# Optimization experiments

Measured on AMD Instinct MI355X. Metric: run time of the kernel, lower is better.

## Reference

```python
import jax, jax.numpy as jnp
import numpy as np

B, C, D = 64, 1000, 2048
SCALE_CONF = 10.0   # confidence scale in forward
SCALE_COS = 16.0    # CosNorm_Classifier default scale


def setup_inputs() -> dict:
    key = jax.random.key(0)
    ks = jax.random.split(key, 8)
    x = jax.random.normal(ks[0], (B, D), jnp.float32)
    labels = jax.random.randint(ks[1], (B,), 0, C)
    centers = jax.random.normal(ks[2], (C, D), jnp.float32)
    class_count = jax.random.randint(ks[3], (C,), 0, 100)
    # learned parameters
    fc_channel_w = jax.random.normal(ks[4], (D, D), jnp.float32) * 0.02
    fc_channel_b = jnp.zeros((D,), jnp.float32)
    fc1_w = jax.random.normal(ks[5], (C, D), jnp.float32) * 0.02
    fc1_b = jnp.zeros((C,), jnp.float32)
    cos_w = jax.random.normal(ks[6], (C, D), jnp.float32) * 0.001
    return {"x": x, "labels": labels, "centers": centers, "class_count": class_count,
            "fc_channel_w": fc_channel_w, "fc_channel_b": fc_channel_b,
            "fc1_w": fc1_w, "fc1_b": fc1_b, "cos_w": cos_w}


def reference(x, labels, centers, class_count, fc_channel_w, fc_channel_b, fc1_w, fc1_b, cos_w):
    # pairwise L2 distance to all class centers; only the per-row min is used
    # downstream, so we fuse the sort-then-take-first into a min reduction.
    x2 = jnp.sum(x * x, axis=1, keepdims=True)            # [B,1]
    c2 = jnp.sum(centers * centers, axis=1)               # [C]
    d2 = jnp.maximum(x2 - 2.0 * (x @ centers.T) + c2[None, :], 0.0)  # [B,C]
    min_dist = jnp.sqrt(jnp.min(d2, axis=1, keepdims=True))          # [B,1] == values_nn[:,0]
    confidence = SCALE_CONF / min_dist                    # broadcasts over feat dim

    # stage-1 classifier -> soft assignment to centers (memory hallucination)
    logits_stage1 = x @ fc1_w.T + fc1_b                   # [B,C]
    prob_stage1 = jax.nn.softmax(logits_stage1, axis=1)
    centers_cur = prob_stage1 @ centers                   # [B,D]

    channel_selector = jnp.tanh(x @ fc_channel_w.T + fc_channel_b)  # [B,D]
    slow_feature = x
    fast_feature = channel_selector * centers_cur
    x_new = confidence * (x + fast_feature)               # [B,D]

    # CosNorm_Classifier: ex = (|x|/(1+|x|)) * x/|x|; ew = w/|w|; logits = scale*ex @ ew.T
    norm_x = jnp.linalg.norm(x_new, axis=1, keepdims=True)
    ex = (norm_x / (1.0 + norm_x)) * (x_new / norm_x)
    ew = cos_w / jnp.linalg.norm(cos_w, axis=1, keepdims=True)
    logits = (SCALE_COS * ex) @ ew.T                      # [B,C]

    return logits, slow_feature, fast_feature
```

## Files before the change

### kernel.cpp

```cpp
#include <hip/hip_runtime.h>
#include <hip/hip_bf16.h>
#include <math.h>

typedef __attribute__((ext_vector_type(8))) short short8;
typedef __attribute__((ext_vector_type(4))) float f32x4;

#define MFMA(a, b, c) __builtin_amdgcn_mfma_f32_16x16x32_bf16(a, b, c, 0, 0, 0)

enum : int {
  WS_XB    = 0,
  WS_X2    = 65536,
  WS_DMINP = 65600,
  WS_SPART = 69696,
  WS_PROB  = 73792,
  WS_SEL   = 106560,
  WS_XNB   = 172096,
  WS_XN2P  = 237632,
  WS_P5    = 245824,
};

__device__ inline short bfs(float f) {
  __hip_bfloat16 h = __float2bfloat16(f);
  return __builtin_bit_cast(short, h);
}
__device__ inline float bf2f(unsigned short u) {
  return __uint_as_float((unsigned)u << 16);
}

__device__ inline void gload16(const float* g, float* lds) {
  __builtin_amdgcn_global_load_lds(
      (const __attribute__((address_space(1))) unsigned int*)g,
      (__attribute__((address_space(3))) unsigned int*)lds, 16, 0, 0);
}

__global__ __launch_bounds__(256) void k1(const float* __restrict__ x,
                                          float* __restrict__ out,
                                          float* __restrict__ ws) {
  __shared__ float red[4];
  int b = blockIdx.x, t = threadIdx.x;
  int l = t & 63, w = t >> 6;
  const float* xr = x + (size_t)b * 2048 + t * 8;
  float4 f0 = *(const float4*)(xr);
  float4 f1 = *(const float4*)(xr + 4);
  short8 h;
  h[0] = bfs(f0.x); h[1] = bfs(f0.y); h[2] = bfs(f0.z); h[3] = bfs(f0.w);
  h[4] = bfs(f1.x); h[5] = bfs(f1.y); h[6] = bfs(f1.z); h[7] = bfs(f1.w);
  *(short8*)((unsigned short*)(ws + WS_XB) + (size_t)b * 2048 + t * 8) = h;
  *(float4*)(out + 64000 + (size_t)b * 2048 + t * 8) = f0;
  *(float4*)(out + 64000 + (size_t)b * 2048 + t * 8 + 4) = f1;
  float s = f0.x*f0.x + f0.y*f0.y + f0.z*f0.z + f0.w*f0.w
          + f1.x*f1.x + f1.y*f1.y + f1.z*f1.z + f1.w*f1.w;
#pragma unroll
  for (int o = 32; o; o >>= 1) s += __shfl_xor(s, o);
  if (l == 0) red[w] = s;
  __syncthreads();
  if (t == 0) ws[WS_X2 + b] = red[0] + red[1] + red[2] + red[3];
}

__global__ __launch_bounds__(512) void k2(const float* __restrict__ centers,
                                          const float* __restrict__ fc1w,
                                          const float* __restrict__ fcw,
                                          const float* __restrict__ fc1b,
                                          const float* __restrict__ fcb,
                                          float* __restrict__ ws) {
  __shared__ float WT[2][16][1028];
  __shared__ f32x4 sacc[8][64];
  __shared__ float ssq[8][64];
  int blk = blockIdx.x, t = threadIdx.x;
  int w = t >> 6, l = t & 63;
  int ln = l & 15, lk = l >> 4;
  int n0 = blk * 16;
  bool cen = (n0 < 1024);

  auto stage = [&](int buf, int koff) {
    for (int r = 0; r < 2; ++r) {
      int row = w * 2 + r;
      int n = n0 + row;
      const float* brow;
      if (n < 1024)      brow = centers + (size_t)min(n, 999) * 2048;
      else if (n < 2048) brow = fc1w + (size_t)min(n - 1024, 999) * 2048;
      else               brow = fcw + (size_t)(n - 2048) * 2048;
#pragma unroll
      for (int j = 0; j < 4; ++j)
        gload16(brow + koff + j * 256 + l * 4, &WT[buf][row][j * 256]);
    }
  };

  stage(0, 0);
  __syncthreads();
  stage(1, 1024);

  int m0 = (w & 3) * 16;
  int kq = (w >> 2) * 512;
  const unsigned short* aptr =
      (const unsigned short*)(ws + WS_XB) + (size_t)(m0 + ln) * 2048 + kq + lk * 8;
  f32x4 acc = {0.f, 0.f, 0.f, 0.f};
  float sq = 0.f;

  {
    const float* wrow = &WT[0][ln][kq + lk * 8];
#pragma unroll 4
    for (int ks = 0; ks < 16; ++ks) {
      short8 a0 = *(const short8*)(aptr + ks * 32);
      float4 f0 = *(const float4*)(wrow + ks * 32);
      float4 f1 = *(const float4*)(wrow + ks * 32 + 4);
      if (cen)
        sq += f0.x*f0.x + f0.y*f0.y + f0.z*f0.z + f0.w*f0.w
            + f1.x*f1.x + f1.y*f1.y + f1.z*f1.z + f1.w*f1.w;
      short8 bb;
      bb[0] = bfs(f0.x); bb[1] = bfs(f0.y); bb[2] = bfs(f0.z); bb[3] = bfs(f0.w);
      bb[4] = bfs(f1.x); bb[5] = bfs(f1.y); bb[6] = bfs(f1.z); bb[7] = bfs(f1.w);
      acc = MFMA(a0, bb, acc);
    }
  }
  __syncthreads();
  {
    const float* wrow = &WT[1][ln][kq + lk * 8];
    const unsigned short* ap1 = aptr + 1024;
#pragma unroll 4
    for (int ks = 0; ks < 16; ++ks) {
      short8 a0 = *(const short8*)(ap1 + ks * 32);
      float4 f0 = *(const float4*)(wrow + ks * 32);
      float4 f1 = *(const float4*)(wrow + ks * 32 + 4);
      if (cen)
        sq += f0.x*f0.x + f0.y*f0.y + f0.z*f0.z + f0.w*f0.w
            + f1.x*f1.x + f1.y*f1.y + f1.z*f1.z + f1.w*f1.w;
      short8 bb;
      bb[0] = bfs(f0.x); bb[1] = bfs(f0.y); bb[2] = bfs(f0.z); bb[3] = bfs(f0.w);
      bb[4] = bfs(f1.x); bb[5] = bfs(f1.y); bb[6] = bfs(f1.z); bb[7] = bfs(f1.w);
      acc = MFMA(a0, bb, acc);
    }
  }

  sacc[w][l] = acc;
  ssq[w][l] = sq;
  __syncthreads();
  if (w < 4) {
    f32x4 a2 = sacc[w + 4][l];
    acc.x += a2.x; acc.y += a2.y; acc.z += a2.z; acc.w += a2.w;
    sq = ssq[w][l] + ssq[w + 4][l];

    if (cen) {
      sq += __shfl_xor(sq, 16);
      sq += __shfl_xor(sq, 32);
      int colv = n0 + ln;
#pragma unroll
      for (int j = 0; j < 4; ++j) {
        int m = m0 + lk * 4 + j;
        float d2 = (colv < 1000)
            ? fmaxf(ws[WS_X2 + m] - 2.f * acc[j] + sq, 0.f) : 3.0e38f;
        d2 = fminf(d2, __shfl_xor(d2, 1));
        d2 = fminf(d2, __shfl_xor(d2, 2));
        d2 = fminf(d2, __shfl_xor(d2, 4));
        d2 = fminf(d2, __shfl_xor(d2, 8));
        if (ln == 0) ws[WS_DMINP + blk * 64 + m] = d2;
      }
    } else if (n0 < 2048) {
      int c = n0 - 1024 + ln;
      unsigned short* pb = (unsigned short*)(ws + WS_PROB);
#pragma unroll
      for (int j = 0; j < 4; ++j) {
        int m = m0 + lk * 4 + j;
        float e = (c < 1000) ? __expf(acc[j] + fc1b[c]) : 0.f;
        pb[(size_t)m * 1024 + c] = (unsigned short)bfs(e);
        float s = e;
        s += __shfl_xor(s, 1);
        s += __shfl_xor(s, 2);
        s += __shfl_xor(s, 4);
        s += __shfl_xor(s, 8);
        if (ln == 0) ws[WS_SPART + (blk - 64) * 64 + m] = s;
      }
    } else {
      int d = n0 - 2048 + ln;
      unsigned short* sel = (unsigned short*)(ws + WS_SEL);
#pragma unroll
      for (int j = 0; j < 4; ++j) {
        int m = m0 + lk * 4 + j;
        float sv = tanhf(acc[j] + fcb[d]);
        sel[(size_t)m * 2048 + d] = (unsigned short)bfs(sv);
      }
    }
  }
}

__global__ __launch_bounds__(256) void kde(const float* __restrict__ centers,
                                           const float* __restrict__ x,
                                           float* __restrict__ out,
                                           float* __restrict__ ws) {
  __shared__ f32x4 sacc[4][2][64];
  __shared__ float sinv[64];
  int blk = blockIdx.x, t = threadIdx.x;
  int w = t >> 6, l = t & 63;
  int cs = blk >> 1, mh = blk & 1;
  int d0 = cs * 16, m0 = mh * 32;
  int ln = l & 15, lk = l >> 4;
  int k0 = w * 256;
  if (t < 64) {
    float s = 0.f;
#pragma unroll
    for (int i = 0; i < 64; ++i) s += ws[WS_SPART + i * 64 + t];
    sinv[t] = 1.0f / s;
  }
  const unsigned short* aptr =
      (const unsigned short*)(ws + WS_PROB) + (size_t)(m0 + ln) * 1024 + k0 + lk * 8;
  f32x4 acc0 = {0.f, 0.f, 0.f, 0.f}, acc1 = {0.f, 0.f, 0.f, 0.f};
  for (int ks = 0; ks < 8; ++ks) {
    short8 a0 = *(const short8*)(aptr + ks * 32);
    short8 a1 = *(const short8*)(aptr + 16 * 1024 + ks * 32);
    int kbase = k0 + ks * 32 + lk * 8;
    short8 bb;
#pragma unroll
    for (int j = 0; j < 8; ++j) {
      int kc = min(kbase + j, 999);
      bb[j] = bfs(centers[(size_t)kc * 2048 + d0 + ln]);
    }
    acc0 = MFMA(a0, bb, acc0);
    acc1 = MFMA(a1, bb, acc1);
  }
  sacc[w][0][l] = acc0;
  sacc[w][1][l] = acc1;
  __syncthreads();
  if (w == 0) {
    f32x4 r0 = sacc[0][0][l], r1 = sacc[0][1][l];
#pragma unroll
    for (int i = 1; i < 4; ++i) {
      f32x4 u0 = sacc[i][0][l], u1 = sacc[i][1][l];
      r0.x += u0.x; r0.y += u0.y; r0.z += u0.z; r0.w += u0.w;
      r1.x += u1.x; r1.y += u1.y; r1.z += u1.z; r1.w += u1.w;
    }
    const unsigned short* sel = (const unsigned short*)(ws + WS_SEL);
    unsigned short* xnb = (unsigned short*)(ws + WS_XNB);
    float rr[8] = {r0.x, r0.y, r0.z, r0.w, r1.x, r1.y, r1.z, r1.w};
#pragma unroll
    for (int q = 0; q < 8; ++q) {
      int b = m0 + (q >> 2) * 16 + lk * 4 + (q & 3);
      int d = d0 + ln;
      float cc = rr[q] * sinv[b];
      float sv = bf2f(sel[(size_t)b * 2048 + d]);
      float xv = x[(size_t)b * 2048 + d];
      float fast = sv * cc;
      out[195072 + (size_t)b * 2048 + d] = fast;
      float yv = xv + fast;
      xnb[(size_t)b * 2048 + d] = (unsigned short)bfs(yv);
      float sq = yv * yv;
      sq += __shfl_xor(sq, 1);
      sq += __shfl_xor(sq, 2);
      sq += __shfl_xor(sq, 4);
      sq += __shfl_xor(sq, 8);
      if (ln == 0) ws[WS_XN2P + cs * 64 + b] = sq;
    }
  }
}

__global__ __launch_bounds__(256) void k7(const float* __restrict__ cosw,
                                          float* __restrict__ ws) {
  int blk = blockIdx.x, t = threadIdx.x;
  int w = t >> 6, l = t & 63;
  int colblk = blk & 31, ksplit = blk >> 5;
  int ln = l & 15, lk = l >> 4;
  int n = colblk * 32 + (w & 1) * 16 + ln;
  int m0 = (w >> 1) * 32;
  int k0 = ksplit * 512;
  const float* bptr = cosw + (size_t)min(n, 999) * 2048 + k0 + lk * 8;
  const unsigned short* aptr =
      (const unsigned short*)(ws + WS_XNB) + (size_t)(m0 + ln) * 2048 + k0 + lk * 8;
  f32x4 acc0 = {0.f, 0.f, 0.f, 0.f}, acc1 = {0.f, 0.f, 0.f, 0.f};
  float sq = 0.f;
#pragma unroll 4
  for (int ks = 0; ks < 16; ++ks) {
    short8 a0 = *(const short8*)(aptr + ks * 32);
    short8 a1 = *(const short8*)(aptr + 16 * 2048 + ks * 32);
    float4 f0 = *(const float4*)(bptr + ks * 32);
    float4 f1 = *(const float4*)(bptr + ks * 32 + 4);
    sq += f0.x*f0.x + f0.y*f0.y + f0.z*f0.z + f0.w*f0.w
        + f1.x*f1.x + f1.y*f1.y + f1.z*f1.z + f1.w*f1.w;
    short8 bb;
    bb[0] = bfs(f0.x); bb[1] = bfs(f0.y); bb[2] = bfs(f0.z); bb[3] = bfs(f0.w);
    bb[4] = bfs(f1.x); bb[5] = bfs(f1.y); bb[6] = bfs(f1.z); bb[7] = bfs(f1.w);
    acc0 = MFMA(a0, bb, acc0);
    acc1 = MFMA(a1, bb, acc1);
  }
  float* P = ws + WS_P5 + ((size_t)ksplit * 1024 + n) * 68;
  *(f32x4*)(P + m0 + lk * 4) = acc0;
  *(f32x4*)(P + m0 + 16 + lk * 4) = acc1;
  sq += __shfl_xor(sq, 16);
  sq += __shfl_xor(sq, 32);
  if (w < 2 && l < 16) P[64] = sq;
}

__global__ __launch_bounds__(256) void k8(float* __restrict__ out,
                                          const float* __restrict__ ws) {
  __shared__ float tile[64][65];
  __shared__ float scale[64];
  int blk = blockIdx.x, t = threadIdx.x, l = t & 63, w = t >> 6;
  int c0 = blk * 64;
  const size_t KS = (size_t)1024 * 68;
  if (t < 64) {
    float s = 0.f;
    for (int i = 0; i < 128; ++i) s += ws[WS_XN2P + i * 64 + t];
    float ny = sqrtf(fmaxf(s, 0.f));
    float d2 = 3.0e38f;
    for (int i = 0; i < 64; ++i) d2 = fminf(d2, ws[WS_DMINP + i * 64 + t]);
    float cf = 10.0f * rsqrtf(fmaxf(d2, 1e-20f));
    scale[t] = 16.0f * cf / (1.0f + cf * ny);
  }
  __syncthreads();
  for (int cl = w; cl < 64; cl += 4) {
    int c = c0 + cl;
    const float* P = ws + WS_P5 + (size_t)c * 68;
    float v = P[l] + P[KS + l] + P[2*KS + l] + P[3*KS + l];
    float w2 = P[64] + P[KS + 64] + P[2*KS + 64] + P[3*KS + 64];
    tile[cl][l] = v * rsqrtf(fmaxf(w2, 1e-30f)) * scale[l];
  }
  __syncthreads();
  for (int r = 0; r < 16; ++r) {
    int b = w * 16 + r;
    int c = c0 + l;
    if (c < 1000) out[(size_t)b * 1000 + c] = tile[l][b];
  }
}

extern "C" void kernel_launch(void* const* d_in, const int* in_sizes, int n_in,
                              void* d_out, int out_size, void* d_ws, size_t ws_size,
                              hipStream_t stream) {
  const float* x       = (const float*)d_in[0];
  const float* centers = (const float*)d_in[2];
  const float* fcw     = (const float*)d_in[4];
  const float* fcb     = (const float*)d_in[5];
  const float* fc1w    = (const float*)d_in[6];
  const float* fc1b    = (const float*)d_in[7];
  const float* cosw    = (const float*)d_in[8];
  float* out = (float*)d_out;
  float* ws  = (float*)d_ws;

  hipLaunchKernelGGL(k1,  dim3(64),  dim3(256), 0, stream, x, out, ws);
  hipLaunchKernelGGL(k2,  dim3(256), dim3(512), 0, stream, centers, fc1w, fcw, fc1b, fcb, ws);
  hipLaunchKernelGGL(kde, dim3(256), dim3(256), 0, stream, centers, x, out, ws);
  hipLaunchKernelGGL(k7,  dim3(128), dim3(256), 0, stream, cosw, ws);
  hipLaunchKernelGGL(k8,  dim3(16),  dim3(256), 0, stream, out, ws);
}
```

Baseline: 67.27 us.

## Pre-transpose centers to bf16 and fuse cosine classifier split-K with finalize

k1 gains extra blocks that transpose the centers matrix into a bf16 [D][1024] buffer. kde can then load contiguous short8 B fragments instead of doing eight strided scalar fp32 loads with a conversion per element. The cosine-classifier GEMM is restructured to 64 blocks of 512 threads that stage cos_w rows in LDS through global_load_lds. Split-K is reduced inside each block and the normalized, scaled logits are written directly, which removes the k8 kernel and its partial-sum buffer. The cost is a transpose pass over centers and fewer, larger blocks in k7.

Result: faster. 58.65 us (-12.8%).

```diff
diff --git a/kernel.cpp b/kernel.cpp
--- a/kernel.cpp
+++ b/kernel.cpp
@@ -16,7 +16,7 @@
   WS_SEL   = 106560,
   WS_XNB   = 172096,
   WS_XN2P  = 237632,
-  WS_P5    = 245824,
+  WS_CTB   = 245824,
 };
 
 __device__ inline short bfs(float f) {
@@ -34,27 +34,46 @@
 }
 
 __global__ __launch_bounds__(256) void k1(const float* __restrict__ x,
+                                          const float* __restrict__ centers,
                                           float* __restrict__ out,
                                           float* __restrict__ ws) {
-  __shared__ float red[4];
-  int b = blockIdx.x, t = threadIdx.x;
+  __shared__ float A[64][65];
+  int blk = blockIdx.x, t = threadIdx.x;
   int l = t & 63, w = t >> 6;
-  const float* xr = x + (size_t)b * 2048 + t * 8;
-  float4 f0 = *(const float4*)(xr);
-  float4 f1 = *(const float4*)(xr + 4);
-  short8 h;
-  h[0] = bfs(f0.x); h[1] = bfs(f0.y); h[2] = bfs(f0.z); h[3] = bfs(f0.w);
-  h[4] = bfs(f1.x); h[5] = bfs(f1.y); h[6] = bfs(f1.z); h[7] = bfs(f1.w);
-  *(short8*)((unsigned short*)(ws + WS_XB) + (size_t)b * 2048 + t * 8) = h;
-  *(float4*)(out + 64000 + (size_t)b * 2048 + t * 8) = f0;
-  *(float4*)(out + 64000 + (size_t)b * 2048 + t * 8 + 4) = f1;
-  float s = f0.x*f0.x + f0.y*f0.y + f0.z*f0.z + f0.w*f0.w
-          + f1.x*f1.x + f1.y*f1.y + f1.z*f1.z + f1.w*f1.w;
-#pragma unroll
-  for (int o = 32; o; o >>= 1) s += __shfl_xor(s, o);
-  if (l == 0) red[w] = s;
-  __syncthreads();
-  if (t == 0) ws[WS_X2 + b] = red[0] + red[1] + red[2] + red[3];
+  if (blk < 64) {
+    int b = blk;
+    const float* xr = x + (size_t)b * 2048 + t * 8;
+    float4 f0 = *(const float4*)(xr);
+    float4 f1 = *(const float4*)(xr + 4);
+    short8 h;
+    h[0] = bfs(f0.x); h[1] = bfs(f0.y); h[2] = bfs(f0.z); h[3] = bfs(f0.w);
+    h[4] = bfs(f1.x); h[5] = bfs(f1.y); h[6] = bfs(f1.z); h[7] = bfs(f1.w);
+    *(short8*)((unsigned short*)(ws + WS_XB) + (size_t)b * 2048 + t * 8) = h;
+    *(float4*)(out + 64000 + (size_t)b * 2048 + t * 8) = f0;
+    *(float4*)(out + 64000 + (size_t)b * 2048 + t * 8 + 4) = f1;
+    float s = f0.x*f0.x + f0.y*f0.y + f0.z*f0.z + f0.w*f0.w
+            + f1.x*f1.x + f1.y*f1.y + f1.z*f1.z + f1.w*f1.w;
+#pragma unroll
+    for (int o = 32; o; o >>= 1) s += __shfl_xor(s, o);
+    if (l == 0) A[0][w] = s;
+    __syncthreads();
+    if (t == 0) ws[WS_X2 + b] = A[0][0] + A[0][1] + A[0][2] + A[0][3];
+  } else {
+    int tid = blk - 64;
+    int tc = tid & 15, td = tid >> 4;
+    int c0 = tc * 64, d0 = td * 64;
+    for (int r = 0; r < 16; ++r) {
+      int cc = r * 4 + w;
+      int c = c0 + cc;
+      A[cc][l] = (c < 1000) ? centers[(size_t)c * 2048 + d0 + l] : 0.f;
+    }
+    __syncthreads();
+    unsigned short* ctb = (unsigned short*)(ws + WS_CTB);
+    for (int r = 0; r < 16; ++r) {
+      int dd = r * 4 + w;
+      ctb[(size_t)(d0 + dd) * 1024 + c0 + l] = (unsigned short)bfs(A[l][dd]);
+    }
+  }
 }
 
 __global__ __launch_bounds__(512) void k2(const float* __restrict__ centers,
@@ -183,8 +202,7 @@
   }
 }
 
-__global__ __launch_bounds__(256) void kde(const float* __restrict__ centers,
-                                           const float* __restrict__ x,
+__global__ __launch_bounds__(256) void kde(const float* __restrict__ x,
                                            float* __restrict__ out,
                                            float* __restrict__ ws) {
   __shared__ f32x4 sacc[4][2][64];
@@ -203,17 +221,14 @@
   }
   const unsigned short* aptr =
       (const unsigned short*)(ws + WS_PROB) + (size_t)(m0 + ln) * 1024 + k0 + lk * 8;
+  const unsigned short* brow =
+      (const unsigned short*)(ws + WS_CTB) + (size_t)(d0 + ln) * 1024 + k0 + lk * 8;
   f32x4 acc0 = {0.f, 0.f, 0.f, 0.f}, acc1 = {0.f, 0.f, 0.f, 0.f};
+#pragma unroll
   for (int ks = 0; ks < 8; ++ks) {
     short8 a0 = *(const short8*)(aptr + ks * 32);
     short8 a1 = *(const short8*)(aptr + 16 * 1024 + ks * 32);
-    int kbase = k0 + ks * 32 + lk * 8;
-    short8 bb;
-#pragma unroll
-    for (int j = 0; j < 8; ++j) {
-      int kc = min(kbase + j, 999);
-      bb[j] = bfs(centers[(size_t)kc * 2048 + d0 + ln]);
-    }
+    short8 bb = *(const short8*)(brow + ks * 32);
     acc0 = MFMA(a0, bb, acc0);
     acc1 = MFMA(a1, bb, acc1);
   }
@@ -252,49 +267,18 @@
   }
 }
 
-__global__ __launch_bounds__(256) void k7(const float* __restrict__ cosw,
+__global__ __launch_bounds__(512) void k7(const float* __restrict__ cosw,
+                                          float* __restrict__ out,
                                           float* __restrict__ ws) {
+  __shared__ float WT[2][16][1028];
+  __shared__ f32x4 sacc[8][64];
+  __shared__ float ssq[8][64];
+  __shared__ float scale_s[64];
   int blk = blockIdx.x, t = threadIdx.x;
   int w = t >> 6, l = t & 63;
-  int colblk = blk & 31, ksplit = blk >> 5;
   int ln = l & 15, lk = l >> 4;
-  int n = colblk * 32 + (w & 1) * 16 + ln;
-  int m0 = (w >> 1) * 32;
-  int k0 = ksplit * 512;
-  const float* bptr = cosw + (size_t)min(n, 999) * 2048 + k0 + lk * 8;
-  const unsigned short* aptr =
-      (const unsigned short*)(ws + WS_XNB) + (size_t)(m0 + ln) * 2048 + k0 + lk * 8;
-  f32x4 acc0 = {0.f, 0.f, 0.f, 0.f}, acc1 = {0.f, 0.f, 0.f, 0.f};
-  float sq = 0.f;
-#pragma unroll 4
-  for (int ks = 0; ks < 16; ++ks) {
-    short8 a0 = *(const short8*)(aptr + ks * 32);
-    short8 a1 = *(const short8*)(aptr + 16 * 2048 + ks * 32);
-    float4 f0 = *(const float4*)(bptr + ks * 32);
-    float4 f1 = *(const float4*)(bptr + ks * 32 + 4);
-    sq += f0.x*f0.x + f0.y*f0.y + f0.z*f0.z + f0.w*f0.w
-        + f1.x*f1.x + f1.y*f1.y + f1.z*f1.z + f1.w*f1.w;
-    short8 bb;
-    bb[0] = bfs(f0.x); bb[1] = bfs(f0.y); bb[2] = bfs(f0.z); bb[3] = bfs(f0.w);
-    bb[4] = bfs(f1.x); bb[5] = bfs(f1.y); bb[6] = bfs(f1.z); bb[7] = bfs(f1.w);
-    acc0 = MFMA(a0, bb, acc0);
-    acc1 = MFMA(a1, bb, acc1);
-  }
-  float* P = ws + WS_P5 + ((size_t)ksplit * 1024 + n) * 68;
-  *(f32x4*)(P + m0 + lk * 4) = acc0;
-  *(f32x4*)(P + m0 + 16 + lk * 4) = acc1;
-  sq += __shfl_xor(sq, 16);
-  sq += __shfl_xor(sq, 32);
-  if (w < 2 && l < 16) P[64] = sq;
-}
-
-__global__ __launch_bounds__(256) void k8(float* __restrict__ out,
-                                          const float* __restrict__ ws) {
-  __shared__ float tile[64][65];
-  __shared__ float scale[64];
-  int blk = blockIdx.x, t = threadIdx.x, l = t & 63, w = t >> 6;
-  int c0 = blk * 64;
-  const size_t KS = (size_t)1024 * 68;
+  int n0 = blk * 16;
+
   if (t < 64) {
     float s = 0.f;
     for (int i = 0; i < 128; ++i) s += ws[WS_XN2P + i * 64 + t];
@@ -302,21 +286,81 @@
     float d2 = 3.0e38f;
     for (int i = 0; i < 64; ++i) d2 = fminf(d2, ws[WS_DMINP + i * 64 + t]);
     float cf = 10.0f * rsqrtf(fmaxf(d2, 1e-20f));
-    scale[t] = 16.0f * cf / (1.0f + cf * ny);
-  }
-  __syncthreads();
-  for (int cl = w; cl < 64; cl += 4) {
-    int c = c0 + cl;
-    const float* P = ws + WS_P5 + (size_t)c * 68;
-    float v = P[l] + P[KS + l] + P[2*KS + l] + P[3*KS + l];
-    float w2 = P[64] + P[KS + 64] + P[2*KS + 64] + P[3*KS + 64];
-    tile[cl][l] = v * rsqrtf(fmaxf(w2, 1e-30f)) * scale[l];
-  }
-  __syncthreads();
-  for (int r = 0; r < 16; ++r) {
-    int b = w * 16 + r;
-    int c = c0 + l;
-    if (c < 1000) out[(size_t)b * 1000 + c] = tile[l][b];
+    scale_s[t] = 16.0f * cf / (1.0f + cf * ny);
+  }
+
+  auto stage = [&](int buf, int koff) {
+    for (int r = 0; r < 2; ++r) {
+      int row = w * 2 + r;
+      const float* brow = cosw + (size_t)min(n0 + row, 999) * 2048;
+#pragma unroll
+      for (int j = 0; j < 4; ++j)
+        gload16(brow + koff + j * 256 + l * 4, &WT[buf][row][j * 256]);
+    }
+  };
+
+  stage(0, 0);
+  __syncthreads();
+  stage(1, 1024);
+
+  int m0 = (w & 3) * 16;
+  int kq = (w >> 2) * 512;
+  const unsigned short* aptr =
+      (const unsigned short*)(ws + WS_XNB) + (size_t)(m0 + ln) * 2048 + kq + lk * 8;
+  f32x4 acc = {0.f, 0.f, 0.f, 0.f};
+  float sq = 0.f;
+
+  {
+    const float* wrow = &WT[0][ln][kq + lk * 8];
+#pragma unroll 4
+    for (int ks = 0; ks < 16; ++ks) {
+      short8 a0 = *(const short8*)(aptr + ks * 32);
+      float4 f0 = *(const float4*)(wrow + ks * 32);
+      float4 f1 = *(const float4*)(wrow + ks * 32 + 4);
+      sq += f0.x*f0.x + f0.y*f0.y + f0.z*f0.z + f0.w*f0.w
+          + f1.x*f1.x + f1.y*f1.y + f1.z*f1.z + f1.w*f1.w;
+      short8 bb;
+      bb[0] = bfs(f0.x); bb[1] = bfs(f0.y); bb[2] = bfs(f0.z); bb[3] = bfs(f0.w);
+      bb[4] = bfs(f1.x); bb[5] = bfs(f1.y); bb[6] = bfs(f1.z); bb[7] = bfs(f1.w);
+      acc = MFMA(a0, bb, acc);
+    }
+  }
+  __syncthreads();
+  {
+    const float* wrow = &WT[1][ln][kq + lk * 8];
+    const unsigned short* ap1 = aptr + 1024;
+#pragma unroll 4
+    for (int ks = 0; ks < 16; ++ks) {
+      short8 a0 = *(const short8*)(ap1 + ks * 32);
+      float4 f0 = *(const float4*)(wrow + ks * 32);
+      float4 f1 = *(const float4*)(wrow + ks * 32 + 4);
+      sq += f0.x*f0.x + f0.y*f0.y + f0.z*f0.z + f0.w*f0.w
+          + f1.x*f1.x + f1.y*f1.y + f1.z*f1.z + f1.w*f1.w;
+      short8 bb;
+      bb[0] = bfs(f0.x); bb[1] = bfs(f0.y); bb[2] = bfs(f0.z); bb[3] = bfs(f0.w);
+      bb[4] = bfs(f1.x); bb[5] = bfs(f1.y); bb[6] = bfs(f1.z); bb[7] = bfs(f1.w);
+      acc = MFMA(a0, bb, acc);
+    }
+  }
+
+  sacc[w][l] = acc;
+  ssq[w][l] = sq;
+  __syncthreads();
+  if (w < 4) {
+    f32x4 a2 = sacc[w + 4][l];
+    acc.x += a2.x; acc.y += a2.y; acc.z += a2.z; acc.w += a2.w;
+    sq = ssq[w][l] + ssq[w + 4][l];
+    sq += __shfl_xor(sq, 16);
+    sq += __shfl_xor(sq, 32);
+    float invw = rsqrtf(fmaxf(sq, 1e-30f));
+    int c = n0 + ln;
+    if (c < 1000) {
+#pragma unroll
+      for (int j = 0; j < 4; ++j) {
+        int m = m0 + lk * 4 + j;
+        out[(size_t)m * 1000 + c] = acc[j] * invw * scale_s[m];
+      }
+    }
   }
 }
 
@@ -333,9 +377,8 @@
   float* out = (float*)d_out;
   float* ws  = (float*)d_ws;
 
-  hipLaunchKernelGGL(k1,  dim3(64),  dim3(256), 0, stream, x, out, ws);
+  hipLaunchKernelGGL(k1,  dim3(576), dim3(256), 0, stream, x, centers, out, ws);
   hipLaunchKernelGGL(k2,  dim3(256), dim3(512), 0, stream, centers, fc1w, fcw, fc1b, fcb, ws);
-  hipLaunchKernelGGL(kde, dim3(256), dim3(256), 0, stream, centers, x, out, ws);
-  hipLaunchKernelGGL(k7,  dim3(128), dim3(256), 0, stream, cosw, ws);
-  hipLaunchKernelGGL(k8,  dim3(16),  dim3(256), 0, stream, out, ws);
-}
+  hipLaunchKernelGGL(kde, dim3(256), dim3(256), 0, stream, x, out, ws);
+  hipLaunchKernelGGL(k7,  dim3(64),  dim3(512), 0, stream, cosw, out, ws);
+}
```
